# Kernel tuning notes

Hardware: AMD Instinct MI355X
Metric: run time of the kernel (lower is better)

## Reference

```python
import jax, jax.numpy as jnp
import numpy as np

DIM = 1536
NH = 12
HD = DIM // NH  # 128
FF, HH, WW = 32, 8, 12
L = FF * HH * WW  # 3072
WIN = (8, 4, 4)  # block of 128 tokens
BLK = WIN[0] * WIN[1] * WIN[2]


def rms_norm(x, g, eps=1e-5):
    # matches RMSNorm: normalize in fp32, scale by weight
    v = jnp.mean(jnp.square(x), axis=-1, keepdims=True)
    return x * jax.lax.rsqrt(v + eps) * g


def rope(x, freqs, n):
    # x: [B,S,D]; freqs: [S,1,HD/2,2] (cos,sin); complex rotation on pairs
    B, S, D = x.shape
    xr = x.reshape(B, S, n, D // n // 2, 2)
    c, s = freqs[..., 0], freqs[..., 1]        # [S,1,HD/2] broadcast over B,n
    a, b = xr[..., 0], xr[..., 1]
    out = jnp.stack([a * c - b * s, a * s + b * c], axis=-1)
    return out.reshape(B, S, D)


def partition3d(x, f, h, w):
    # [B,f,h,w,D] -> [B, nblocks, 128, D], block order (f/8, h/4, w/4)
    B, D = x.shape[0], x.shape[-1]
    wf, wh, ww = WIN
    x = x.reshape(B, f // wf, wf, h // wh, wh, w // ww, ww, D)
    x = x.transpose(0, 1, 3, 5, 2, 4, 6, 7)
    return x.reshape(B, -1, BLK, D)


def reverse3d(xw, f, h, w):
    # [B, nblocks, 128, D] -> [B, f*h*w, D]
    B, D = xw.shape[0], xw.shape[-1]
    wf, wh, ww = WIN
    x = xw.reshape(B, f // wf, h // wh, w // ww, wf, wh, ww, D)
    x = x.transpose(0, 1, 4, 2, 5, 3, 6, 7)
    return x.reshape(B, f * h * w, D)


def block_mask(f, h, w):
    # build_local_block_mask_3d: spatial mask is all-ones; temporal = context|local
    seqlen = f // WIN[0]
    nb_sp = (h // WIN[1]) * (w // WIN[2])
    stride = WIN[0]
    ctx_idx = (6 + stride - 1) // stride - 1          # context_frames=6
    radius = (5 + stride - 1) // stride               # temp_window_frames=5
    t = jnp.arange(seqlen)
    mt = (t[None, :] <= ctx_idx) | (jnp.abs(t[:, None] - t[None, :]) <= radius)
    # expand temporal block mask over spatial blocks -> [nb, nb]
    return jnp.repeat(jnp.repeat(mt, nb_sp, axis=0), nb_sp, axis=1)


def setup_inputs() -> dict:
    key = jax.random.key(0)
    ks = jax.random.split(key, 8)
    x = jax.random.normal(ks[0], (1, L, DIM), jnp.float32)
    ang = jax.random.uniform(ks[1], (L, 1, HD // 2), jnp.float32, 0.0, 2.0 * np.pi)
    freqs = jnp.stack([jnp.cos(ang), jnp.sin(ang)], axis=-1)  # [L,1,64,2]
    sc = 1.0 / np.sqrt(DIM)
    Wq = jax.random.normal(ks[2], (DIM, DIM), jnp.float32) * sc
    Wk = jax.random.normal(ks[3], (DIM, DIM), jnp.float32) * sc
    Wv = jax.random.normal(ks[4], (DIM, DIM), jnp.float32) * sc
    Wo = jax.random.normal(ks[5], (DIM, DIM), jnp.float32) * sc
    zeros = jnp.zeros((DIM,), jnp.float32)
    ones = jnp.ones((DIM,), jnp.float32)
    return {"x": x, "freqs": freqs, "Wq": Wq, "bq": zeros, "Wk": Wk, "bk": zeros,
            "Wv": Wv, "bv": zeros, "Wo": Wo, "bo": zeros, "g_q": ones, "g_k": ones,
            "f": FF, "h": HH, "w": WW, "local_range": 18}


def reference(x, freqs, Wq, bq, Wk, bk, Wv, bv, Wo, bo, g_q, g_k, f, h, w, local_range):
    B, S, D = x.shape
    q = rms_norm(x @ Wq + bq, g_q, eps=1e-5)
    k = rms_norm(x @ Wk + bk, g_k, eps=1e-5)
    v = x @ Wv + bv
    q = rope(q, freqs, NH)
    k = rope(k, freqs, NH)
    # window partition and flatten back to a reordered sequence
    qs = partition3d(q.reshape(B, f, h, w, D), f, h, w).reshape(B, S, D)
    ks_ = partition3d(k.reshape(B, f, h, w, D), f, h, w).reshape(B, S, D)
    vs = partition3d(v.reshape(B, f, h, w, D), f, h, w).reshape(B, S, D)
    bm = block_mask(f, h, w)                       # [nb, nb] bool
    tok_mask = jnp.repeat(jnp.repeat(bm, BLK, 0), BLK, 1)  # [S, S]
    qh = qs.reshape(B, S, NH, HD).transpose(0, 2, 1, 3)
    kh = ks_.reshape(B, S, NH, HD).transpose(0, 2, 1, 3)
    vh = vs.reshape(B, S, NH, HD).transpose(0, 2, 1, 3)
    scores = jnp.einsum('bhqd,bhkd->bhqk', qh, kh) / np.sqrt(HD)
    scores = jnp.where(tok_mask[None, None], scores, -jnp.inf)
    attn = jax.nn.softmax(scores, axis=-1)
    out = jnp.einsum('bhqk,bhkd->bhqd', attn, vh)
    out = out.transpose(0, 2, 1, 3).reshape(B, S, D)
    out = reverse3d(out.reshape(B, -1, BLK, D), f, h, w)  # undo window reorder
    return out @ Wo + bo
```

## Files before the change

kernel.cpp:

```cpp
#include <hip/hip_runtime.h>
#include <hip/hip_bf16.h>
#include <math.h>

#define S_LEN 3072
#define DMODEL 1536
#define NQKV 4608
#define NHEAD 12
#define HDIM 128
#define NSPLIT 4

typedef __attribute__((ext_vector_type(8))) short bf16x8;
typedef __attribute__((ext_vector_type(4))) float f32x4;
typedef __attribute__((ext_vector_type(4))) unsigned int u32x4;

__device__ __forceinline__ void gload_lds16(const void* g, void* lds) {
  __builtin_amdgcn_global_load_lds(
      (const __attribute__((address_space(1))) unsigned int*)g,
      (__attribute__((address_space(3))) unsigned int*)lds, 16, 0, 0);
}

__device__ __forceinline__ int invperm(int p) {
  int blk = p >> 7;
  int w   = p & 127;
  int fb  = blk / 6;
  int rem = blk - fb * 6;
  int hb  = rem / 3;
  int wb  = rem - hb * 3;
  int fi  = fb * 8 + (w >> 4);
  int hi  = hb * 4 + ((w >> 2) & 3);
  int wi  = wb * 4 + (w & 3);
  return (fi * 8 + hi) * 12 + wi;
}

__device__ __forceinline__ int fwdperm(int s) {
  int fi = s / 96;
  int rem = s - fi * 96;
  int hi = rem / 12;
  int wi = rem - hi * 12;
  int fb = fi >> 3, wf = fi & 7;
  int hb = hi >> 2, wh = hi & 3;
  int wb = wi >> 2, ww = wi & 3;
  return ((fb * 2 + hb) * 3 + wb) * 128 + wf * 16 + wh * 4 + ww;
}

__device__ __forceinline__ void store_out(float* p, float v) { *p = v; }
__device__ __forceinline__ void store_out(__hip_bfloat16* p, float v) { *p = __float2bfloat16(v); }

__global__ __launch_bounds__(256) void convert_bias(
    const float* __restrict__ in, __hip_bfloat16* __restrict__ out,
    const float* __restrict__ bq, const float* __restrict__ bk,
    const float* __restrict__ bv, float* __restrict__ bqkv)
{
  if (blockIdx.x < 4608) {
    int i = blockIdx.x * 256 + threadIdx.x;
    float4 v = ((const float4*)in)[i];
    __hip_bfloat16 b[4] = {__float2bfloat16(v.x), __float2bfloat16(v.y),
                           __float2bfloat16(v.z), __float2bfloat16(v.w)};
    ((ushort4*)out)[i] = *(ushort4*)b;
  } else {
    int j = (blockIdx.x - 4608) * 256 + threadIdx.x;
    float v = (j < 1536) ? bq[j] : (j < 3072) ? bk[j - 1536] : bv[j - 3072];
    bqkv[j] = v;
  }
}

__global__ __launch_bounds__(256) void transpose_convert4(
    const float* __restrict__ W0, const float* __restrict__ W1,
    const float* __restrict__ W2, const float* __restrict__ W3,
    __hip_bfloat16* __restrict__ Wtqkv, __hip_bfloat16* __restrict__ Wot)
{
  __shared__ __hip_bfloat16 Ls[64][67];
  const int z = blockIdx.z;
  const float* W = (z == 0) ? W0 : (z == 1) ? W1 : (z == 2) ? W2 : W3;
  __hip_bfloat16* Wt = (z < 3) ? Wtqkv + (size_t)z * DMODEL * DMODEL : Wot;
  const int r0 = blockIdx.y * 64, c0 = blockIdx.x * 64, t = threadIdx.x;
  {
    int rr = t >> 2, cb = (t & 3) * 16;
    const float4* src = (const float4*)(W + (size_t)(r0 + rr) * DMODEL + c0 + cb);
    #pragma unroll
    for (int i = 0; i < 4; ++i) {
      float4 v = src[i];
      Ls[rr][cb + i * 4 + 0] = __float2bfloat16(v.x);
      Ls[rr][cb + i * 4 + 1] = __float2bfloat16(v.y);
      Ls[rr][cb + i * 4 + 2] = __float2bfloat16(v.z);
      Ls[rr][cb + i * 4 + 3] = __float2bfloat16(v.w);
    }
  }
  __syncthreads();
  {
    int cc = t >> 2, rb = (t & 3) * 16;
    unsigned short tmp[16];
    #pragma unroll
    for (int i = 0; i < 16; ++i) tmp[i] = *(unsigned short*)&Ls[rb + i][cc];
    uint4* dst = (uint4*)(Wt + (size_t)(c0 + cc) * DMODEL + r0 + rb);
    dst[0] = ((uint4*)tmp)[0];
    dst[1] = ((uint4*)tmp)[1];
  }
}

template <typename OutT, int BN>
__global__ __launch_bounds__(256) void gemm_bt(
    const __hip_bfloat16* __restrict__ A, const __hip_bfloat16* __restrict__ Bt,
    const float* __restrict__ bias, OutT* __restrict__ C, int M, int N, int K)
{
  constexpr int NB = BN / 32;
  __shared__ __hip_bfloat16 As[128 * 64];
  __shared__ __hip_bfloat16 Bs[BN * 64];
  const int tid = threadIdx.x, lane = tid & 63, wid = tid >> 6;
  const int l15 = lane & 15, l4 = lane >> 4;
  const int lin = blockIdx.y * gridDim.x + blockIdx.x;
  const int xcd = lin & 7, idx = lin >> 3;
  const int CX = gridDim.x >> 2, CY = gridDim.y >> 1;
  const int cx = xcd & 3, cy = xcd >> 2;
  const int lc = idx % CX, lr = idx / CX;
  const int row0 = (cy * CY + lr) * 128, col0 = (cx * CX + lc) * BN;
  const int wr = (wid >> 1) * 64, wc = (wid & 1) * (BN / 2);

  f32x4 acc[4][NB] = {};
  const char* Ab = (const char*)A;
  const char* Bb = (const char*)Bt;

  auto STAGE = [&](int k0) {
    #pragma unroll
    for (int i = 0; i < 4; ++i) {
      int slot = i * 256 + tid;
      int r = slot >> 3;
      int b = ((slot & 7) * 16) ^ ((r & 7) << 4);
      gload_lds16(Ab + ((size_t)(row0 + r) * K + k0) * 2 + b,
                  (char*)As + slot * 16);
    }
    #pragma unroll
    for (int i = 0; i < BN / 32; ++i) {
      int slot = i * 256 + tid;
      int r = slot >> 3;
      int b = ((slot & 7) * 16) ^ ((r & 7) << 4);
      gload_lds16(Bb + ((size_t)(col0 + r) * K + k0) * 2 + b,
                  (char*)Bs + slot * 16);
    }
  };

  for (int k0 = 0; k0 < K; k0 += 64) {
    STAGE(k0);
    __syncthreads();
    #pragma unroll
    for (int kk = 0; kk < 2; ++kk) {
      bf16x8 a[4], b[NB];
      #pragma unroll
      for (int m = 0; m < 4; ++m) {
        int row = wr + m * 16 + l15;
        int byte = (kk * 64 + l4 * 16) ^ ((row & 7) << 4);
        a[m] = *(const bf16x8*)((const char*)As + row * 128 + byte);
      }
      #pragma unroll
      for (int n = 0; n < NB; ++n) {
        int row = wc + n * 16 + l15;
        int byte = (kk * 64 + l4 * 16) ^ ((row & 7) << 4);
        b[n] = *(const bf16x8*)((const char*)Bs + row * 128 + byte);
      }
      #pragma unroll
      for (int m = 0; m < 4; ++m)
        #pragma unroll
        for (int n = 0; n < NB; ++n)
          acc[m][n] = __builtin_amdgcn_mfma_f32_16x16x32_bf16(a[m], b[n], acc[m][n], 0, 0, 0);
    }
    __syncthreads();
  }

  #pragma unroll
  for (int m = 0; m < 4; ++m) {
    #pragma unroll
    for (int r = 0; r < 4; ++r) {
      size_t row = row0 + wr + m * 16 + l4 * 4 + r;
      #pragma unroll
      for (int n = 0; n < NB; ++n) {
        int col = col0 + wc + n * 16 + l15;
        store_out(&C[row * N + col], acc[m][n][r] + bias[col]);
      }
    }
  }
}

__global__ __launch_bounds__(256) void norm_rope_perm(
    const __hip_bfloat16* __restrict__ X,
    const float* __restrict__ gq, const float* __restrict__ gk,
    const float* __restrict__ freqs,
    __hip_bfloat16* __restrict__ OutQ, __hip_bfloat16* __restrict__ OutK)
{
  const int s = blockIdx.x, tid = threadIdx.x;
  const int sec = blockIdx.y;
  const float* g = sec ? gk : gq;
  __hip_bfloat16* Out = sec ? OutK : OutQ;
  const float qsc = sec ? 1.0f : (0.08838834764831843f * 1.4426950408889634f);
  const unsigned int* row = (const unsigned int*)(X + (size_t)s * NQKV + sec * 1536);
  float e0[3], e1[3];
  float ss = 0.f;
  #pragma unroll
  for (int i = 0; i < 3; ++i) {
    unsigned int u = row[tid + i * 256];
    float a = __uint_as_float(u << 16);
    float b = __uint_as_float(u & 0xffff0000u);
    e0[i] = a; e1[i] = b;
    ss += a * a + b * b;
  }
  #pragma unroll
  for (int off = 32; off > 0; off >>= 1) ss += __shfl_down(ss, off, 64);
  __shared__ float wsum[4];
  if ((tid & 63) == 0) wsum[tid >> 6] = ss;
  __syncthreads();
  float rs = rsqrtf((wsum[0] + wsum[1] + wsum[2] + wsum[3]) * (1.f / DMODEL) + 1e-5f);
  rs *= qsc;
  const int p = fwdperm(s);
  #pragma unroll
  for (int i = 0; i < 3; ++i) {
    int pi = tid + i * 256;
    int n = pi >> 6, d2 = pi & 63;
    float c  = freqs[(size_t)s * 128 + 2 * d2];
    float sn = freqs[(size_t)s * 128 + 2 * d2 + 1];
    float y0 = e0[i] * rs * g[2 * pi];
    float y1 = e1[i] * rs * g[2 * pi + 1];
    float o0 = y0 * c - y1 * sn;
    float o1 = y0 * sn + y1 * c;
    __hip_bfloat16 b0 = __float2bfloat16(o0), b1 = __float2bfloat16(o1);
    unsigned int u = ((unsigned int)(*(unsigned short*)&b1) << 16) | (*(unsigned short*)&b0);
    ((unsigned int*)Out)[(((size_t)n * S_LEN + p) * HDIM + 2 * d2) >> 1] = u;
  }
}

__global__ __launch_bounds__(256) void v_transpose(
    const __hip_bfloat16* __restrict__ Vsec, __hip_bfloat16* __restrict__ Vt)
{
  __shared__ __hip_bfloat16 Ls[64][136];
  const int p0 = blockIdx.x * 64, h = blockIdx.y, t = threadIdx.x;
  {
    int pl = t & 63, dg = t >> 6;
    int sidx = invperm(p0 + pl);
    const uint4* src = (const uint4*)(Vsec + (size_t)sidx * NQKV + h * HDIM + dg * 32);
    #pragma unroll
    for (int i = 0; i < 4; ++i) {
      uint4 v = src[i];
      *(uint4*)&Ls[pl][dg * 32 + i * 8] = v;
    }
  }
  __syncthreads();
  {
    int d = t >> 1, ph = t & 1;
    unsigned short tmp[32];
    #pragma unroll
    for (int i = 0; i < 32; ++i) tmp[i] = *(unsigned short*)&Ls[ph * 32 + i][d];
    uint4* dst = (uint4*)(Vt + ((size_t)h * HDIM + d) * S_LEN + p0 + ph * 32);
    #pragma unroll
    for (int i = 0; i < 4; ++i) dst[i] = ((uint4*)tmp)[i];
  }
}

__global__ __launch_bounds__(512) void attn_mfma(
    const __hip_bfloat16* __restrict__ Qp, const __hip_bfloat16* __restrict__ Kp,
    const __hip_bfloat16* __restrict__ Vt,
    __hip_bfloat16* __restrict__ Opart, float* __restrict__ ml)
{
  __shared__ __hip_bfloat16 Ks[64 * 128];
  __shared__ __hip_bfloat16 Vs[128 * 64];

  const int hw = blockIdx.x + 24 * (blockIdx.y + NSPLIT * blockIdx.z);
  const int L  = (hw & 7) * 144 + (hw >> 3);
  const int j  = L % 6;
  const int t4 = (L / 6) & 3;
  const int sh = L / 24;
  const int h  = sh % 12;
  const int split = sh / 12;
  const int tg = (t4 == 0) ? 2 : (t4 == 1) ? 1 : (t4 == 2) ? 3 : 0;
  const int qb = tg * 6 + j;

  const int tid = threadIdx.x, lane = tid & 63, wid = tid >> 6;
  const int l15 = lane & 15, l4 = lane >> 4;

  const int NCh = (tg == 0) ? 6 : (tg == 2) ? 12 : 9;
  const int cbegin = split * NCh, cend = cbegin + NCh;

  const char* Kh = (const char*)(Kp + (size_t)h * S_LEN * HDIM);
  const char* Vh = (const char*)(Vt + (size_t)h * HDIM * S_LEN);

  const int kbase = 8 * (l15 >> 2) + (l15 & 3);
  const int ksw = (((l15 & 3) | (((l15 >> 2) & 1) << 2))) << 4;

  unsigned int koffA, voffA;
  {
    unsigned int kr = tid >> 4;
    unsigned int sig = (kr & 3) | (((kr >> 3) & 1) << 2);
    koffA = kr * 256 + (((tid & 15) * 16) ^ (sig << 4));
    unsigned int vr = tid >> 3;
    voffA = vr * (S_LEN * 2) + (((tid & 7) * 16) ^ ((vr & 7) << 4));
  }

  auto k0_of = [&](int ci) { return ci * 64 + ((tg == 3 && ci >= 12) ? 768 : 0); };
  auto STAGE = [&](int k0) {
    const char* ks = Kh + (size_t)k0 * 256;
    gload_lds16(ks + koffA,        (char*)Ks + tid * 16);
    gload_lds16(ks + koffA + 8192, (char*)Ks + tid * 16 + 8192);
    const char* vs = Vh + (size_t)k0 * 2 + voffA;
    gload_lds16(vs,                          (char*)Vs + tid * 16);
    gload_lds16(vs + (size_t)64 * S_LEN * 2, (char*)Vs + tid * 16 + 8192);
  };

  bf16x8 aq[4];
  {
    const __hip_bfloat16* qr = Qp + (size_t)h * S_LEN * HDIM
        + (size_t)(qb * 128 + wid * 16 + l15) * HDIM + l4 * 8;
    #pragma unroll
    for (int dc = 0; dc < 4; ++dc) aq[dc] = *(const bf16x8*)(qr + dc * 32);
  }

  f32x4 oacc[8] = {};
  float m2 = -1e30f;
  float lsum = 0.f;

  for (int ci = cbegin; ci < cend; ++ci) {
    const int k0 = k0_of(ci);
    STAGE(k0);
    __syncthreads();

    f32x4 sfr[4] = {};
    __builtin_amdgcn_s_setprio(1);
    #pragma unroll
    for (int ct = 0; ct < 4; ++ct) {
      int key = kbase + (ct >> 1) * 32 + (ct & 1) * 4;
      #pragma unroll
      for (int dc = 0; dc < 4; ++dc) {
        int b = (dc * 64 + l4 * 16) ^ ksw;
        bf16x8 kf = *(const bf16x8*)((const char*)Ks + key * 256 + b);
        sfr[ct] = __builtin_amdgcn_mfma_f32_16x16x32_bf16(kf, aq[dc], sfr[ct], 0, 0, 0);
      }
    }
    __builtin_amdgcn_s_setprio(0);
    float lmax = fmaxf(
        fmaxf(fmaxf(sfr[0][0], sfr[0][1]), fmaxf(sfr[0][2], sfr[0][3])),
        fmaxf(fmaxf(fmaxf(sfr[1][0], sfr[1][1]), fmaxf(sfr[1][2], sfr[1][3])),
              fmaxf(fmaxf(fmaxf(sfr[2][0], sfr[2][1]), fmaxf(sfr[2][2], sfr[2][3])),
                    fmaxf(fmaxf(sfr[3][0], sfr[3][1]), fmaxf(sfr[3][2], sfr[3][3])))));
    bool grow = lmax > m2 + 8.f;
    if (ci == cbegin || __any(grow)) {
      float mf = lmax;
      mf = fmaxf(mf, __shfl_xor(mf, 16, 64));
      mf = fmaxf(mf, __shfl_xor(mf, 32, 64));
      float mn = fmaxf(m2, mf);
      float corr = exp2f(m2 - mn);
      m2 = mn;
      lsum *= corr;
      float cr[4];
      #pragma unroll
      for (int r = 0; r < 4; ++r) cr[r] = __shfl(corr, l4 * 4 + r, 64);
      #pragma unroll
      for (int n = 0; n < 8; ++n)
        #pragma unroll
        for (int r = 0; r < 4; ++r) oacc[n][r] *= cr[r];
    }
    #pragma unroll
    for (int ct = 0; ct < 4; ++ct)
      #pragma unroll
      for (int r = 0; r < 4; ++r) {
        float p = exp2f(sfr[ct][r] - m2);
        sfr[ct][r] = p;
        lsum += p;
      }
    #pragma unroll
    for (int ks = 0; ks < 2; ++ks) {
      u32x4 wv;
      {
        __hip_bfloat16 a0 = __float2bfloat16(sfr[2 * ks][0]);
        __hip_bfloat16 a1 = __float2bfloat16(sfr[2 * ks][1]);
        __hip_bfloat16 a2 = __float2bfloat16(sfr[2 * ks][2]);
        __hip_bfloat16 a3 = __float2bfloat16(sfr[2 * ks][3]);
        __hip_bfloat16 b0 = __float2bfloat16(sfr[2 * ks + 1][0]);
        __hip_bfloat16 b1 = __float2bfloat16(sfr[2 * ks + 1][1]);
        __hip_bfloat16 b2 = __float2bfloat16(sfr[2 * ks + 1][2]);
        __hip_bfloat16 b3 = __float2bfloat16(sfr[2 * ks + 1][3]);
        wv[0] = ((unsigned int)(*(unsigned short*)&a1) << 16) | (*(unsigned short*)&a0);
        wv[1] = ((unsigned int)(*(unsigned short*)&a3) << 16) | (*(unsigned short*)&a2);
        wv[2] = ((unsigned int)(*(unsigned short*)&b1) << 16) | (*(unsigned short*)&b0);
        wv[3] = ((unsigned int)(*(unsigned short*)&b3) << 16) | (*(unsigned short*)&b2);
      }
      bf16x8 pa = __builtin_bit_cast(bf16x8, wv);
      __builtin_amdgcn_s_setprio(1);
      #pragma unroll
      for (int n = 0; n < 8; ++n) {
        int d = n * 16 + l15;
        int b = (ks * 64 + l4 * 16) ^ ((d & 7) << 4);
        bf16x8 bv = *(const bf16x8*)((const char*)Vs + d * 128 + b);
        oacc[n] = __builtin_amdgcn_mfma_f32_16x16x32_bf16(pa, bv, oacc[n], 0, 0, 0);
      }
      __builtin_amdgcn_s_setprio(0);
    }
    __syncthreads();
  }

  float t = lsum;
  t += __shfl_xor(t, 16, 64);
  t += __shfl_xor(t, 32, 64);
  float inv = 1.0f / t;
  #pragma unroll
  for (int r = 0; r < 4; ++r) {
    float invr = __shfl(inv, l4 * 4 + r, 64);
    int qrow = qb * 128 + wid * 16 + l4 * 4 + r;
    size_t rowid = (size_t)(split * NHEAD + h) * S_LEN + qrow;
    __hip_bfloat16* dst = Opart + rowid * HDIM;
    #pragma unroll
    for (int n = 0; n < 8; ++n)
      dst[n * 16 + l15] = __float2bfloat16(oacc[n][r] * invr);
  }
  if (lane < 16) {
    int qrow = qb * 128 + wid * 16 + lane;
    size_t rowid = (size_t)(split * NHEAD + h) * S_LEN + qrow;
    ml[rowid * 2 + 0] = m2;
    ml[rowid * 2 + 1] = t;
  }
}

__global__ __launch_bounds__(256) void attn_merge(
    const __hip_bfloat16* __restrict__ Opart, const float* __restrict__ ml,
    __hip_bfloat16* __restrict__ AO)
{
  const int rid = blockIdx.x * 4 + (threadIdx.x >> 6);
  const int lane = threadIdx.x & 63;
  const int h = rid / S_LEN, q = rid - h * S_LEN;
  size_t rr[NSPLIT];
  float m[NSPLIT], l[NSPLIT];
  float mm = -1e30f;
  #pragma unroll
  for (int s = 0; s < NSPLIT; ++s) {
    rr[s] = (size_t)(s * NHEAD + h) * S_LEN + q;
    m[s] = ml[rr[s] * 2];
    l[s] = ml[rr[s] * 2 + 1];
    mm = fmaxf(mm, m[s]);
  }
  float wsum = 0.f, wgt[NSPLIT];
  #pragma unroll
  for (int s = 0; s < NSPLIT; ++s) { wgt[s] = l[s] * exp2f(m[s] - mm); wsum += wgt[s]; }
  float inv = 1.0f / wsum;
  float o0 = 0.f, o1 = 0.f;
  #pragma unroll
  for (int s = 0; s < NSPLIT; ++s) {
    unsigned int u = ((const unsigned int*)(Opart + rr[s] * HDIM))[lane];
    float a = wgt[s] * inv;
    o0 += a * __uint_as_float(u << 16);
    o1 += a * __uint_as_float(u & 0xffff0000u);
  }
  __hip_bfloat16 b0 = __float2bfloat16(o0), b1 = __float2bfloat16(o1);
  unsigned int u = ((unsigned int)(*(unsigned short*)&b1) << 16) | (*(unsigned short*)&b0);
  int sorig = invperm(q);
  ((unsigned int*)(AO + (size_t)sorig * DMODEL + h * HDIM))[lane] = u;
}

extern "C" void kernel_launch(void* const* d_in, const int* in_sizes, int n_in,
                              void* d_out, int out_size, void* d_ws, size_t ws_size,
                              hipStream_t stream)
{
  (void)in_sizes; (void)n_in; (void)out_size; (void)ws_size;
  const float* x     = (const float*)d_in[0];
  const float* freqs = (const float*)d_in[1];
  const float* Wq    = (const float*)d_in[2];
  const float* bq    = (const float*)d_in[3];
  const float* Wk    = (const float*)d_in[4];
  const float* bk    = (const float*)d_in[5];
  const float* Wv    = (const float*)d_in[6];
  const float* bv    = (const float*)d_in[7];
  const float* Wo    = (const float*)d_in[8];
  const float* bo    = (const float*)d_in[9];
  const float* gq    = (const float*)d_in[10];
  const float* gk    = (const float*)d_in[11];
  float* out = (float*)d_out;

  char* w = (char*)d_ws;
  __hip_bfloat16* xbf    = (__hip_bfloat16*)(w);
  __hip_bfloat16* Wtqkv  = (__hip_bfloat16*)(w + 9437184);
  __hip_bfloat16* QKVbf  = (__hip_bfloat16*)(w + 23592960);
  __hip_bfloat16* Qp     = (__hip_bfloat16*)(w + 51904512);
  __hip_bfloat16* Kp     = (__hip_bfloat16*)(w + 61341696);
  __hip_bfloat16* Vtb    = (__hip_bfloat16*)(w + 70778880);
  __hip_bfloat16* AO     = (__hip_bfloat16*)(w + 80216064);
  __hip_bfloat16* Wot    = (__hip_bfloat16*)(w + 89653248);
  float*          bqkv   = (float*)(w + 94371840);
  __hip_bfloat16* Opart  = (__hip_bfloat16*)(w + 9437184);
  float*          mlbuf  = (float*)(w);

  hipLaunchKernelGGL(convert_bias, dim3(4626), dim3(256), 0, stream,
                     x, xbf, bq, bk, bv, bqkv);
  hipLaunchKernelGGL(transpose_convert4, dim3(24, 24, 4), dim3(256), 0, stream,
                     Wq, Wk, Wv, Wo, Wtqkv, Wot);

  hipLaunchKernelGGL((gemm_bt<__hip_bfloat16, 64>), dim3(NQKV / 64, S_LEN / 128),
                     dim3(256), 0, stream, xbf, Wtqkv, bqkv, QKVbf, S_LEN, NQKV, DMODEL);

  hipLaunchKernelGGL(norm_rope_perm, dim3(S_LEN, 2), dim3(256), 0, stream,
                     QKVbf, gq, gk, freqs, Qp, Kp);
  hipLaunchKernelGGL(v_transpose, dim3(48, 12), dim3(256), 0, stream, QKVbf + 3072, Vtb);

  hipLaunchKernelGGL(attn_mfma, dim3(24, NSPLIT, NHEAD), dim3(512), 0, stream,
                     Qp, Kp, Vtb, Opart, mlbuf);
  hipLaunchKernelGGL(attn_merge, dim3(S_LEN * NHEAD / 4), dim3(256), 0, stream,
                     Opart, mlbuf, AO);

  hipLaunchKernelGGL((gemm_bt<float, 64>), dim3(DMODEL / 64, S_LEN / 128),
                     dim3(256), 0, stream, AO, Wot, bo, out, S_LEN, DMODEL, DMODEL);
}
```

Measured before the change: 201.9 us.

## Use fixed 12-chunk attention splits with variable split count per query group

```diff
diff --git a/kernel.cpp b/kernel.cpp
--- a/kernel.cpp
+++ b/kernel.cpp
@@ -261,21 +261,22 @@
   __shared__ __hip_bfloat16 Ks[64 * 128];
   __shared__ __hip_bfloat16 Vs[128 * 64];
 
-  const int hw = blockIdx.x + 24 * (blockIdx.y + NSPLIT * blockIdx.z);
-  const int L  = (hw & 7) * 144 + (hw >> 3);
+  const int hw = blockIdx.x;
+  const int L  = (hw & 7) * 108 + (hw >> 3);
   const int j  = L % 6;
-  const int t4 = (L / 6) & 3;
-  const int sh = L / 24;
-  const int h  = sh % 12;
-  const int split = sh / 12;
-  const int tg = (t4 == 0) ? 2 : (t4 == 1) ? 1 : (t4 == 2) ? 3 : 0;
+  const int c  = (L / 6) % 12;
+  const int h  = L / 72;
+  int tg, split;
+  if (c < 2)      { tg = 0; split = c; }
+  else if (c < 5) { tg = 1; split = c - 2; }
+  else if (c < 9) { tg = 2; split = c - 5; }
+  else            { tg = 3; split = c - 9; }
   const int qb = tg * 6 + j;
 
   const int tid = threadIdx.x, lane = tid & 63, wid = tid >> 6;
   const int l15 = lane & 15, l4 = lane >> 4;
 
-  const int NCh = (tg == 0) ? 6 : (tg == 2) ? 12 : 9;
-  const int cbegin = split * NCh, cend = cbegin + NCh;
+  const int cbegin = split * 12, cend = cbegin + 12;
 
   const char* Kh = (const char*)(Kp + (size_t)h * S_LEN * HDIM);
   const char* Vh = (const char*)(Vt + (size_t)h * HDIM * S_LEN);
@@ -422,23 +423,22 @@
   const int rid = blockIdx.x * 4 + (threadIdx.x >> 6);
   const int lane = threadIdx.x & 63;
   const int h = rid / S_LEN, q = rid - h * S_LEN;
+  const int tg = q / 768;
+  const int nsp = (tg == 0) ? 2 : (tg == 2) ? 4 : 3;
   size_t rr[NSPLIT];
   float m[NSPLIT], l[NSPLIT];
   float mm = -1e30f;
-  #pragma unroll
-  for (int s = 0; s < NSPLIT; ++s) {
+  for (int s = 0; s < nsp; ++s) {
     rr[s] = (size_t)(s * NHEAD + h) * S_LEN + q;
     m[s] = ml[rr[s] * 2];
     l[s] = ml[rr[s] * 2 + 1];
     mm = fmaxf(mm, m[s]);
   }
   float wsum = 0.f, wgt[NSPLIT];
-  #pragma unroll
-  for (int s = 0; s < NSPLIT; ++s) { wgt[s] = l[s] * exp2f(m[s] - mm); wsum += wgt[s]; }
+  for (int s = 0; s < nsp; ++s) { wgt[s] = l[s] * exp2f(m[s] - mm); wsum += wgt[s]; }
   float inv = 1.0f / wsum;
   float o0 = 0.f, o1 = 0.f;
-  #pragma unroll
-  for (int s = 0; s < NSPLIT; ++s) {
+  for (int s = 0; s < nsp; ++s) {
     unsigned int u = ((const unsigned int*)(Opart + rr[s] * HDIM))[lane];
     float a = wgt[s] * inv;
     o0 += a * __uint_as_float(u << 16);
@@ -494,7 +494,7 @@
                      QKVbf, gq, gk, freqs, Qp, Kp);
   hipLaunchKernelGGL(v_transpose, dim3(48, 12), dim3(256), 0, stream, QKVbf + 3072, Vtb);
 
-  hipLaunchKernelGGL(attn_mfma, dim3(24, NSPLIT, NHEAD), dim3(512), 0, stream,
+  hipLaunchKernelGGL(attn_mfma, dim3(864), dim3(512), 0, stream,
                      Qp, Kp, Vtb, Opart, mlbuf);
   hipLaunchKernelGGL(attn_merge, dim3(S_LEN * NHEAD / 4), dim3(256), 0, stream,
                      Opart, mlbuf, AO);
```

Result: slower. 208.5 us (+3.2%).
